# Kernel optimization log

Measured on AMD Instinct MI355X. Metric: run time of the kernel, lower is better.

Reference implementation:

```python
import jax, jax.numpy as jnp
import numpy as np

B, C, D, E = 2048, 64, 1024, 128
P_INT = 0.0  # p_int=0 -> intervention mask is all zeros (deterministic)


def setup_inputs() -> dict:
    key = jax.random.key(0)
    ks = jax.random.split(key, 16)
    s = lambda k, shape, fan: jax.random.normal(k, shape, jnp.float32) * (1.0 / np.sqrt(fan))
    return {
        "x": jax.random.normal(ks[0], (B, D), jnp.float32),
        "c_int": jax.random.uniform(ks[1], (B, C), jnp.float32),
        # stacked per-concept scorer MLP: Linear(D,D) -> ReLU -> Linear(D,1) -> Sigmoid
        "W1": s(ks[2], (C, D, D), D), "b1": jnp.zeros((C, D), jnp.float32),
        "w2": s(ks[3], (C, D), D), "b2": jnp.zeros((C,), jnp.float32),
        # stacked per-concept embed layer: Linear(D+1, D+1) -> ReLU
        "Wl": s(ks[4], (C, D + 1, D + 1), D + 1), "bl": jnp.zeros((C, D + 1), jnp.float32),
        # shared heads
        "Wmu": s(ks[5], (D + 1, E), D + 1), "bmu": jnp.zeros((E,), jnp.float32),
        "Wlv": s(ks[6], (D + 1, E), D + 1), "blv": jnp.zeros((E,), jnp.float32),
        "proto_pos": jax.random.normal(ks[7], (C, E), jnp.float32),
        "proto_neg": jax.random.normal(ks[8], (C, E), jnp.float32),
    }


def reference(x, c_int, W1, b1, w2, b2, Wl, bl, Wmu, bmu, Wlv, blv, proto_pos, proto_neg):
    # Concept scorers (all concepts batched as one grouped GEMM).
    h = jax.nn.relu(jnp.einsum("bd,cdk->bck", x, W1) + b1)          # [B,C,D]
    c_pred = jax.nn.sigmoid(jnp.einsum("bck,ck->bc", h, w2) + b2)    # [B,C]
    # Per-concept embedding layer on [x ; c_pred].
    xc = jnp.concatenate(
        [jnp.broadcast_to(x[:, None, :], (x.shape[0], C, D)), c_pred[..., None]], axis=-1
    )                                                                # [B,C,D+1]
    emb = jax.nn.relu(jnp.einsum("bck,ckj->bcj", xc, Wl) + bl)       # [B,C,D+1]
    mu = jnp.einsum("bcj,je->bce", emb, Wmu) + bmu                   # [B,C,E]
    logvar = jnp.einsum("bcj,je->bce", emb, Wlv) + blv               # [B,C,E]
    c_emb = mu  # eval mode: no reparameterization noise
    # Intervention blend (mask ~ Bernoulli(p_int); p_int=0 -> zeros, deterministic)
    mask = jnp.zeros_like(c_pred)                                    # [B,C]
    cp = mask * c_int + (1.0 - mask) * c_pred                        # [B,C]
    proto = cp[..., None] * proto_pos + (1.0 - cp[..., None]) * proto_neg  # [B,C,E]
    c_emb = mask[..., None] * proto + (1.0 - mask[..., None]) * c_emb
    return (c_pred, c_emb, mu, logvar)
```

## Files before the change

kernel.cpp:

```cpp
#include <hip/hip_runtime.h>
#include <hip/hip_bf16.h>
#include <cstdint>
#include <cstddef>

#define OFF_CE 131072ull
#define OFF_MU (131072ull + 16777216ull)
#define OFF_LV (131072ull + 33554432ull)

using bf16x8 = __attribute__((ext_vector_type(8))) __bf16;
using s16x8  = __attribute__((ext_vector_type(8))) short;
using f32x4  = __attribute__((ext_vector_type(4))) float;

__device__ __forceinline__ unsigned short f2bf(float x) {
  unsigned u = __builtin_bit_cast(unsigned, x);
  return (unsigned short)((u + 0x7FFFu + ((u >> 16) & 1u)) >> 16);
}
__device__ __forceinline__ float bf2f(unsigned short h) {
  unsigned u = ((unsigned)h) << 16;
  return __builtin_bit_cast(float, u);
}
__device__ __forceinline__ void async16(const void* g, void* l) {
  __builtin_amdgcn_global_load_lds(
      (const __attribute__((address_space(1))) void*)g,
      (__attribute__((address_space(3))) void*)l, 16, 0, 0);
}

struct P {
  const float *Wl, *bl, *Wmu, *Wlv, *b2;
  const unsigned short *xb;
  unsigned short *WlT, *WheadT;
  float *wlastf, *blpf, *Wlcolf, *w2l, *bl1024, *whead1024f, *presum, *spart, *e1024, *pred;
};

__device__ __forceinline__ void strip_transpose(const float* __restrict__ srcBase, int srcStride,
                                                unsigned short* __restrict__ dstBase, int tid,
                                                char* lds) {
  float* t64 = (float*)lds;
  const int r = tid >> 3;
  const int c8 = (tid & 7) << 3;
  for (int nc = 0; nc < 16; ++nc) {
    __syncthreads();
    const float* sp = srcBase + (size_t)r * srcStride + nc * 64 + c8;
#pragma unroll
    for (int j = 0; j < 8; ++j) t64[r * 65 + c8 + j] = sp[j];
    __syncthreads();
    unsigned short tmp[8];
#pragma unroll
    for (int j = 0; j < 8; ++j) tmp[j] = f2bf(t64[(c8 + j) * 65 + r]);
    *(uint4*)(dstBase + (size_t)(nc * 64 + r) * 1024 + c8) = *(uint4*)tmp;
  }
}

__global__ __launch_bounds__(512) void prep1_k(const float* __restrict__ W1,
                                               const float* __restrict__ x,
                                               const float* __restrict__ Wl,
                                               const float* __restrict__ bl,
                                               unsigned short* __restrict__ xb,
                                               unsigned short* __restrict__ W1T,
                                               float* __restrict__ wlastf,
                                               float* __restrict__ blpf,
                                               float* __restrict__ Wlcolf,
                                               float* __restrict__ w2l,
                                               float* __restrict__ bl1024) {
  __shared__ char lds[16640];
  const int bid = blockIdx.x;
  const int tid = threadIdx.x;
  if (bid < 1024) {
    const int c = bid & 63, k0 = (bid >> 6) << 6;
    strip_transpose(W1 + ((size_t)c << 20) + (size_t)k0 * 1024, 1024,
                    W1T + ((size_t)c << 20) + k0, tid, lds);
  } else if (bid < 1536) {
    const int idx = (bid - 1024) * 512 + tid;
    const float4* xv = (const float4*)x;
    float4 a = xv[idx * 2], b = xv[idx * 2 + 1];
    unsigned w0 = f2bf(a.x) | ((unsigned)f2bf(a.y) << 16);
    unsigned w1 = f2bf(a.z) | ((unsigned)f2bf(a.w) << 16);
    unsigned w2 = f2bf(b.x) | ((unsigned)f2bf(b.y) << 16);
    unsigned w3 = f2bf(b.z) | ((unsigned)f2bf(b.w) << 16);
    ((uint4*)xb)[idx] = make_uint4(w0, w1, w2, w3);
  } else {
    const int idx = (bid - 1536) * 512 + tid;
    const int c = idx >> 10, j = idx & 1023;
    const float* src = Wl + (size_t)c * 1050625;
    wlastf[idx] = src[(size_t)1024 * 1025 + j];
    blpf[idx]   = bl[(size_t)c * 1025 + j];
    Wlcolf[idx] = src[(size_t)j * 1025 + 1024];
    if (j == 0) {
      w2l[c]    = src[(size_t)1024 * 1025 + 1024];
      bl1024[c] = bl[(size_t)c * 1025 + 1024];
    }
  }
}

__global__ __launch_bounds__(512) void transpose_wl_strip_k(const float* __restrict__ Wl,
                                                            unsigned short* __restrict__ WlT) {
  __shared__ char lds[16640];
  const int bid = blockIdx.x;
  const int c = bid & 63, k0 = (bid >> 6) << 6;
  strip_transpose(Wl + (size_t)c * 1050625 + (size_t)k0 * 1025, 1025,
                  WlT + ((size_t)c << 20) + k0, threadIdx.x, lds);
}

template <int FUSE_WL>
__device__ void extra_work(int e, int tid, char* lds, const P& p) {
  if constexpr (FUSE_WL) {
    if (e < 1024) {
      const int c = e & 63, k0 = (e >> 6) << 6;
      strip_transpose(p.Wl + (size_t)c * 1050625 + (size_t)k0 * 1025, 1025,
                      p.WlT + ((size_t)c << 20) + k0, tid, lds);
      return;
    }
    e -= 1024;
  }
  if (e < 512) {
    const int idx = e * 512 + tid;
    const int rr = idx >> 10, k = idx & 1023;
    float v = (rr < 128) ? p.Wmu[(size_t)k * 128 + rr] : p.Wlv[(size_t)k * 128 + (rr - 128)];
    p.WheadT[idx] = f2bf(v);
    if (e == 0 && tid < 256)
      p.whead1024f[tid] = (tid < 128) ? p.Wmu[131072 + tid] : p.Wlv[131072 + (tid - 128)];
    return;
  }
  e -= 512;
  const int r0 = e << 5;
  uint4* xt4 = (uint4*)lds;
  const uint4* src4 = (const uint4*)(p.xb + ((size_t)r0 << 10));
#pragma unroll
  for (int i = 0; i < 8; ++i) xt4[tid * 8 + i] = src4[tid * 8 + i];
  __syncthreads();
  const int wv = tid >> 6, lane = tid & 63;
  const unsigned short* xt = (const unsigned short*)lds;
  for (int c = 0; c < 64; ++c) {
    float w[16];
#pragma unroll
    for (int q = 0; q < 16; ++q) w[q] = p.Wlcolf[(c << 10) + lane * 16 + q];
#pragma unroll
    for (int rr = 0; rr < 4; ++rr) {
      const int r = (wv << 2) + rr;
      const unsigned short* xr = xt + (r << 10) + lane * 16;
      float s = 0.f;
#pragma unroll
      for (int i = 0; i < 16; ++i) s += bf2f(xr[i]) * w[i];
#pragma unroll
      for (int off = 32; off; off >>= 1) s += __shfl_xor(s, off);
      if (lane == 0) p.presum[(c << 11) + r0 + r] = s;
    }
  }
}


#define BAR() __builtin_amdgcn_s_barrier()
#define LGKM0() do { asm volatile("s_waitcnt lgkmcnt(0)" ::: "memory"); \
                     __builtin_amdgcn_sched_barrier(0); } while (0)
#define VM4() asm volatile("s_waitcnt vmcnt(4)" ::: "memory")
#define VM0() asm volatile("s_waitcnt vmcnt(0)" ::: "memory")

#define STAGEA(h, tt, bidx) do { _Pragma("unroll") for (int q_ = 0; q_ < 2; ++q_) \
  async16(Asrc[q_] + ((size_t)(h) * 128) * K + (size_t)(tt) * 64, \
          &sA[bidx][(h) * 8192 + chnk[q_]]); } while (0)
#define STAGEB(h, tt, bidx) do { _Pragma("unroll") for (int q_ = 0; q_ < 2; ++q_) \
  async16(Bsrc[q_] + ((size_t)(h) * 128) * K + (size_t)(tt) * 64, \
          &sB[bidx][(h) * 8192 + chnk[q_]]); } while (0)

#define LOADA(mh, bidx) do { _Pragma("unroll") for (int i_ = 0; i_ < 4; ++i_) { \
  const int ro_ = ((mh) * 128 + wm64 + i_ * 16 + l15) << 6; \
  a[i_][0] = *(const bf16x8*)&sA[bidx][ro_ + ccx0]; \
  a[i_][1] = *(const bf16x8*)&sA[bidx][ro_ + ccx1]; } } while (0)

#define LOADB(nh, bb, bidx) do { _Pragma("unroll") for (int j_ = 0; j_ < 2; ++j_) { \
  const int ro_ = ((nh) * 128 + wn32 + j_ * 16 + l15) << 6; \
  bb[j_][0] = *(const bf16x8*)&sB[bidx][ro_ + ccx0]; \
  bb[j_][1] = *(const bf16x8*)&sB[bidx][ro_ + ccx1]; } } while (0)

#define MMAQ(mh, nh, bb) do { _Pragma("unroll") for (int i_ = 0; i_ < 4; ++i_) \
  _Pragma("unroll") for (int j_ = 0; j_ < 2; ++j_) { \
    acc[(mh)*4+i_][(nh)*2+j_] = __builtin_amdgcn_mfma_f32_16x16x32_bf16( \
        a[i_][0], bb[j_][0], acc[(mh)*4+i_][(nh)*2+j_], 0, 0, 0); \
    acc[(mh)*4+i_][(nh)*2+j_] = __builtin_amdgcn_mfma_f32_16x16x32_bf16( \
        a[i_][1], bb[j_][1], acc[(mh)*4+i_][(nh)*2+j_], 0, 0, 0); \
  } } while (0)

template <int MODE, int FUSE_WL>
__global__ __launch_bounds__(512, 2) void gemm8p_k(
    const unsigned short* __restrict__ A, const unsigned short* __restrict__ BT, const int K,
    const float* __restrict__ e0, const float* __restrict__ e1,
    const float* __restrict__ e2, const float* __restrict__ e3,
    unsigned short* __restrict__ obf, float* __restrict__ ofl, P p) {
  __shared__ unsigned short sA[2][16384];
  __shared__ unsigned short sB[2][16384];

  constexpr int GX = (MODE == 2) ? 1 : 4;
  constexpr int GY = (MODE == 2) ? 512 : 8;
  constexpr int NWG = GX * GY * ((MODE == 2) ? 1 : 64);

  const int tid = threadIdx.x;

  int rbid;
  if constexpr (MODE == 0) {
    constexpr int NE = FUSE_WL ? 1600 : 576;
    constexpr int NT = 2048 + NE;
    const int bidR = blockIdx.x;
    const int lo = (int)(((long)bidR * NE) / NT);
    const int hi = (int)(((long)(bidR + 1) * NE) / NT);
    if (hi > lo) { extra_work<FUSE_WL>(lo, tid, (char*)&sA[0][0], p); return; }
    rbid = bidR - lo;
  } else {
    rbid = blockIdx.x + GX * (blockIdx.y + GY * blockIdx.z);
  }

  const int lane = tid & 63;
  const int wid = tid >> 6;
  const int wm = wid >> 2, wn = wid & 3;
  const int l15 = lane & 15, l4 = lane >> 4;
  const int wm64 = wm << 6, wn32 = wn << 5;

  const int bid = (rbid & 7) * (NWG >> 3) + (rbid >> 3);
  const int bx = bid % GX;
  const int by = (bid / GX) % GY;
  const int c = bid / (GX * GY);

  const int n0 = bx << 8;
  const int m0 = by << 8;

  const unsigned short* Ab = A;
  const unsigned short* Bb;
  if constexpr (MODE == 2) Bb = BT;
  else                     Bb = BT + ((size_t)c << 20);

  int rloc[2], csrc[2], chnk[2];
  const unsigned short* Asrc[2];
  const unsigned short* Bsrc[2];
#pragma unroll
  for (int q = 0; q < 2; ++q) {
    const int s = ((wid << 1) + q) * 64 + lane;
    rloc[q] = s >> 3;
    csrc[q] = ((s & 7) ^ ((s >> 3) & 7)) << 3;
    chnk[q] = ((wid << 1) + q) << 9;
    Asrc[q] = Ab + (size_t)(m0 + rloc[q]) * K + csrc[q];
    Bsrc[q] = Bb + (size_t)(n0 + rloc[q]) * K + csrc[q];
  }

  const int xorv = l15 & 7;
  const int ccx0 = (l4 ^ xorv) << 3;
  const int ccx1 = ((4 + l4) ^ xorv) << 3;

  f32x4 acc[8][4];
#pragma unroll
  for (int i = 0; i < 8; ++i)
#pragma unroll
    for (int j = 0; j < 4; ++j) acc[i][j] = (f32x4)(0.f);

  bf16x8 a[4][2], b0[2][2], b1[2][2];

  const int nt = K >> 6;

  STAGEA(0, 0, 0); STAGEB(0, 0, 0); STAGEB(1, 0, 0); STAGEA(1, 0, 0);
  VM0();
  BAR();

  for (int t = 0; t < nt - 1; ++t) {
    const int cb = t & 1, nb = cb ^ 1;
    LOADA(0, cb);
    LOADB(0, b0, cb);
    STAGEA(0, t + 1, nb);
    BAR();
    LGKM0();
    __builtin_amdgcn_s_setprio(1);
    MMAQ(0, 0, b0);
    __builtin_amdgcn_s_setprio(0);
    VM4();
    BAR();
    LOADB(1, b1, cb);
    STAGEB(0, t + 1, nb);
    BAR();
    LGKM0();
    __builtin_amdgcn_s_setprio(1);
    MMAQ(0, 1, b1);
    __builtin_amdgcn_s_setprio(0);
    VM4();
    BAR();
    LOADA(1, cb);
    STAGEB(1, t + 1, nb);
    BAR();
    LGKM0();
    __builtin_amdgcn_s_setprio(1);
    MMAQ(1, 1, b1);
    __builtin_amdgcn_s_setprio(0);
    BAR();
    STAGEA(1, t + 1, nb);
    BAR();
    __builtin_amdgcn_s_setprio(1);
    MMAQ(1, 0, b0);
    __builtin_amdgcn_s_setprio(0);
    VM4();
    BAR();
  }

  {
    const int cb = (nt - 1) & 1;
    VM0();
    BAR();
    LOADA(0, cb);
    LOADB(0, b0, cb);
    LGKM0();
    __builtin_amdgcn_s_setprio(1);
    MMAQ(0, 0, b0);
    __builtin_amdgcn_s_setprio(0);
    LOADB(1, b1, cb);
    LGKM0();
    __builtin_amdgcn_s_setprio(1);
    MMAQ(0, 1, b1);
    __builtin_amdgcn_s_setprio(0);
    LOADA(1, cb);
    LGKM0();
    __builtin_amdgcn_s_setprio(1);
    MMAQ(1, 1, b1);
    MMAQ(1, 0, b0);
    __builtin_amdgcn_s_setprio(0);
  }

  int coln[2][2];
#pragma unroll
  for (int nh = 0; nh < 2; ++nh)
#pragma unroll
    for (int j = 0; j < 2; ++j) coln[nh][j] = n0 + nh * 128 + wn32 + j * 16 + l15;

  if constexpr (MODE == 0) {
    float bias[2][2], w2v[2][2];
#pragma unroll
    for (int nh = 0; nh < 2; ++nh)
#pragma unroll
      for (int j = 0; j < 2; ++j) {
        bias[nh][j] = e0[(c << 10) + coln[nh][j]];
        w2v[nh][j]  = e1[(c << 10) + coln[nh][j]];
      }
    float* partL = (float*)&sA[0][0];
#pragma unroll
    for (int mh = 0; mh < 2; ++mh)
#pragma unroll
      for (int i = 0; i < 4; ++i)
#pragma unroll
        for (int rr = 0; rr < 4; ++rr) {
          float s = 0.f;
#pragma unroll
          for (int nh = 0; nh < 2; ++nh)
#pragma unroll
            for (int j = 0; j < 2; ++j) {
              float v = fmaxf(acc[mh * 4 + i][nh * 2 + j][rr] + bias[nh][j], 0.f);
              s += v * w2v[nh][j];
            }
          s += __shfl_xor(s, 1); s += __shfl_xor(s, 2);
          s += __shfl_xor(s, 4); s += __shfl_xor(s, 8);
          if (l15 == 0) partL[wid * 128 + mh * 64 + i * 16 + (l4 << 2) + rr] = s;
        }
    __syncthreads();
    if (tid < 256) {
      const int r = tid;
      const int mh_ = r >> 7, wmr = (r >> 6) & 1, low = r & 63;
      float s2 = 0.f;
#pragma unroll
      for (int wn2 = 0; wn2 < 4; ++wn2) s2 += partL[(wmr * 4 + wn2) * 128 + mh_ * 64 + low];
      ofl[(((size_t)(bx << 6) + c) << 11) + m0 + r] = s2;
    }
  } else if constexpr (MODE == 1) {
    float* cpL = (float*)&sA[0][0];
    if (tid < 256) {
      const int b = m0 + tid;
      float s = p.b2[c];
#pragma unroll
      for (int q = 0; q < 4; ++q) s += e2[(((size_t)(q << 6) + c) << 11) + b];
      float pv = 1.f / (1.f + expf(-s));
      cpL[tid] = pv;
      if (bx == 0) {
        p.pred[((size_t)b << 6) + c] = pv;
        p.e1024[(c << 11) + b] =
            fmaxf(p.presum[(c << 11) + b] + pv * p.w2l[c] + p.bl1024[c], 0.f);
      }
    }
    __syncthreads();
    float wl4[2][2], bb4[2][2];
#pragma unroll
    for (int nh = 0; nh < 2; ++nh)
#pragma unroll
      for (int j = 0; j < 2; ++j) {
        wl4[nh][j] = e0[(c << 10) + coln[nh][j]];
        bb4[nh][j] = e1[(c << 10) + coln[nh][j]];
      }
#pragma unroll
    for (int mh = 0; mh < 2; ++mh)
#pragma unroll
      for (int i = 0; i < 4; ++i)
#pragma unroll
        for (int rr = 0; rr < 4; ++rr) {
          const int rl = mh * 128 + wm64 + i * 16 + (l4 << 2) + rr;
          const int row = m0 + rl;
          const float cp = cpL[rl];
          unsigned short* orow = obf + (((size_t)(c << 11) + row) << 10);
#pragma unroll
          for (int nh = 0; nh < 2; ++nh)
#pragma unroll
            for (int j = 0; j < 2; ++j) {
              float v = acc[mh * 4 + i][nh * 2 + j][rr] + cp * wl4[nh][j] + bb4[nh][j];
              orow[coln[nh][j]] = f2bf(fmaxf(v, 0.f));
            }
        }
  } else {
    float bias[2][2], wh[2][2];
#pragma unroll
    for (int nh = 0; nh < 2; ++nh)
#pragma unroll
      for (int j = 0; j < 2; ++j) {
        bias[nh][j] = (nh == 0) ? e0[coln[0][j]] : e1[coln[1][j] - 128];
        wh[nh][j]   = e3[coln[nh][j]];
      }
#pragma unroll
    for (int mh = 0; mh < 2; ++mh)
#pragma unroll
      for (int i = 0; i < 4; ++i)
#pragma unroll
        for (int rr = 0; rr < 4; ++rr) {
          const int rid = m0 + mh * 128 + wm64 + i * 16 + (l4 << 2) + rr;
          const int cc = rid >> 11, b = rid & 2047;
          const float ev = e2[rid];
          const size_t ib = (((size_t)b << 6) + cc) << 7;
#pragma unroll
          for (int j = 0; j < 2; ++j) {
            float v = acc[mh * 4 + i][j][rr] + bias[0][j] + ev * wh[0][j];
            ofl[OFF_MU + ib + coln[0][j]] = v;
            ofl[OFF_CE + ib + coln[0][j]] = v;
          }
#pragma unroll
          for (int j = 0; j < 2; ++j) {
            float v = acc[mh * 4 + i][2 + j][rr] + bias[1][j] + ev * wh[1][j];
            ofl[OFF_LV + ib + (coln[1][j] - 128)] = v;
          }
        }
  }
}


extern "C" void kernel_launch(void* const* d_in, const int* in_sizes, int n_in,
                              void* d_out, int out_size, void* d_ws, size_t ws_size,
                              hipStream_t stream) {
  const float* x   = (const float*)d_in[0];
  const float* W1  = (const float*)d_in[2];
  const float* b1  = (const float*)d_in[3];
  const float* w2  = (const float*)d_in[4];
  const float* b2  = (const float*)d_in[5];
  const float* Wl  = (const float*)d_in[6];
  const float* bl  = (const float*)d_in[7];
  const float* Wmu = (const float*)d_in[8];
  const float* bmu = (const float*)d_in[9];
  const float* Wlv = (const float*)d_in[10];
  const float* blv = (const float*)d_in[11];
  float* out = (float*)d_out;

  const bool fuse = ws_size >= 545523712ull;

  char* ws = (char*)d_ws;
  size_t off = 0;
  auto take = [&](size_t bytes) { char* r = ws + off; off += bytes; return r; };
  unsigned short* xb     = (unsigned short*)take(4194304);
  unsigned short* W1T    = (unsigned short*)take(134217728);
  unsigned short* WlT    = fuse ? (unsigned short*)take(134217728) : W1T;
  float* wlastf          = (float*)take(262144);
  float* blpf            = (float*)take(262144);
  float* Wlcolf          = (float*)take(262144);
  float* w2l             = (float*)take(512);
  float* bl1024          = (float*)take(512);
  unsigned short* WheadT = (unsigned short*)take(524288);
  float* whead1024f      = (float*)take(1024);
  float* presum          = (float*)take(524288);
  float* spart           = (float*)take(2097152);
  float* e1024f          = (float*)take(524288);
  unsigned short* emb    = (unsigned short*)take(268435456);

  P p;
  p.Wl = Wl; p.bl = bl; p.Wmu = Wmu; p.Wlv = Wlv; p.b2 = b2;
  p.xb = xb; p.WlT = WlT; p.WheadT = WheadT;
  p.wlastf = wlastf; p.blpf = blpf; p.Wlcolf = Wlcolf; p.w2l = w2l; p.bl1024 = bl1024;
  p.whead1024f = whead1024f; p.presum = presum; p.spart = spart;
  p.e1024 = e1024f; p.pred = out;

  prep1_k<<<1664, 512, 0, stream>>>(W1, x, Wl, bl, xb, W1T, wlastf, blpf, Wlcolf, w2l, bl1024);
  if (fuse) {
    gemm8p_k<0, 1><<<2048 + 1600, 512, 0, stream>>>(xb, W1T, 1024, b1, w2, nullptr, nullptr,
                                                    nullptr, spart, p);
  } else {
    gemm8p_k<0, 0><<<2048 + 576, 512, 0, stream>>>(xb, W1T, 1024, b1, w2, nullptr, nullptr,
                                                   nullptr, spart, p);
    transpose_wl_strip_k<<<1024, 512, 0, stream>>>(Wl, WlT);
  }
  gemm8p_k<1, 0><<<dim3(4, 8, 64), 512, 0, stream>>>(xb, WlT, 1024, wlastf, blpf, spart, nullptr,
                                                     emb, nullptr, p);
  gemm8p_k<2, 0><<<dim3(1, 512, 1), 512, 0, stream>>>(emb, WheadT, 1024, bmu, blv, e1024f,
                                                      whead1024f, nullptr, out, p);
}
```

Measured before the change: 1.137 ms.

## Replace strip transposes with 64x64 tile kernels and unfuse extra work from GEMM

Weight transposes now use one 256-thread block per 64x64 tile with float4 loads (for W1), replacing the serial 16-step strip loop. The extra work that used to be interleaved into the first GEMM grid (Wl transpose, head weight transpose, presum dot products) moves to a separate wl2_k kernel launched between the two grouped GEMMs. This lets one transposed-weight buffer be reused for W1 and Wl. presum is recomputed with one block per row using vector loads. The cost is losing the overlap of transpose work with GEMM compute, in exchange for better-parallelised, more coalesced transposes.

```diff
diff --git a/kernel.cpp b/kernel.cpp
--- a/kernel.cpp
+++ b/kernel.cpp
@@ -25,33 +25,41 @@
       (__attribute__((address_space(3))) void*)l, 16, 0, 0);
 }
 
-struct P {
-  const float *Wl, *bl, *Wmu, *Wlv, *b2;
-  const unsigned short *xb;
-  unsigned short *WlT, *WheadT;
-  float *wlastf, *blpf, *Wlcolf, *w2l, *bl1024, *whead1024f, *presum, *spart, *e1024, *pred;
+struct P2 {
+  const float *b2, *presum, *w2l, *bl1024;
+  float *e1024, *pred;
 };
 
-__device__ __forceinline__ void strip_transpose(const float* __restrict__ srcBase, int srcStride,
-                                                unsigned short* __restrict__ dstBase, int tid,
-                                                char* lds) {
-  float* t64 = (float*)lds;
-  const int r = tid >> 3;
-  const int c8 = (tid & 7) << 3;
-  for (int nc = 0; nc < 16; ++nc) {
-    __syncthreads();
-    const float* sp = srcBase + (size_t)r * srcStride + nc * 64 + c8;
-#pragma unroll
-    for (int j = 0; j < 8; ++j) t64[r * 65 + c8 + j] = sp[j];
-    __syncthreads();
+template <int ALIGNED>
+__device__ __forceinline__ void tile_tr64(const float* __restrict__ src, int stride,
+                                          unsigned short* __restrict__ dst, int tid,
+                                          float (*t)[68]) {
+#pragma unroll
+  for (int i = 0; i < 4; ++i) {
+    const int row = (tid >> 4) + (i << 4);
+    const int col4 = (tid & 15) << 2;
+    const float* sp = src + (size_t)row * stride + col4;
+    float4 v;
+    if constexpr (ALIGNED) {
+      v = *(const float4*)sp;
+    } else {
+      v.x = sp[0]; v.y = sp[1]; v.z = sp[2]; v.w = sp[3];
+    }
+    *(float4*)&t[row][col4] = v;
+  }
+  __syncthreads();
+  const int n = tid & 63;
+#pragma unroll
+  for (int p = 0; p < 2; ++p) {
+    const int k8 = ((tid >> 6) << 3) + (p << 5);
     unsigned short tmp[8];
 #pragma unroll
-    for (int j = 0; j < 8; ++j) tmp[j] = f2bf(t64[(c8 + j) * 65 + r]);
-    *(uint4*)(dstBase + (size_t)(nc * 64 + r) * 1024 + c8) = *(uint4*)tmp;
-  }
-}
-
-__global__ __launch_bounds__(512) void prep1_k(const float* __restrict__ W1,
+    for (int j = 0; j < 8; ++j) tmp[j] = f2bf(t[k8 + j][n]);
+    *(uint4*)(dst + (size_t)n * 1024 + k8) = *(uint4*)tmp;
+  }
+}
+
+__global__ __launch_bounds__(256) void prep1_k(const float* __restrict__ W1,
                                                const float* __restrict__ x,
                                                const float* __restrict__ Wl,
                                                const float* __restrict__ bl,
@@ -62,15 +70,15 @@
                                                float* __restrict__ Wlcolf,
                                                float* __restrict__ w2l,
                                                float* __restrict__ bl1024) {
-  __shared__ char lds[16640];
+  __shared__ float t[64][68];
   const int bid = blockIdx.x;
   const int tid = threadIdx.x;
-  if (bid < 1024) {
-    const int c = bid & 63, k0 = (bid >> 6) << 6;
-    strip_transpose(W1 + ((size_t)c << 20) + (size_t)k0 * 1024, 1024,
-                    W1T + ((size_t)c << 20) + k0, tid, lds);
-  } else if (bid < 1536) {
-    const int idx = (bid - 1024) * 512 + tid;
+  if (bid < 16384) {
+    const int c = bid >> 8, kt = (bid >> 4) & 15, nt = bid & 15;
+    tile_tr64<1>(W1 + ((size_t)c << 20) + ((size_t)(kt << 6) << 10) + (nt << 6), 1024,
+                 W1T + ((size_t)c << 20) + ((size_t)(nt << 6) << 10) + (kt << 6), tid, t);
+  } else if (bid < 17408) {
+    const int idx = (bid - 16384) * 256 + tid;
     const float4* xv = (const float4*)x;
     float4 a = xv[idx * 2], b = xv[idx * 2 + 1];
     unsigned w0 = f2bf(a.x) | ((unsigned)f2bf(a.y) << 16);
@@ -79,7 +87,7 @@
     unsigned w3 = f2bf(b.z) | ((unsigned)f2bf(b.w) << 16);
     ((uint4*)xb)[idx] = make_uint4(w0, w1, w2, w3);
   } else {
-    const int idx = (bid - 1536) * 512 + tid;
+    const int idx = (bid - 17408) * 256 + tid;
     const int c = idx >> 10, j = idx & 1023;
     const float* src = Wl + (size_t)c * 1050625;
     wlastf[idx] = src[(size_t)1024 * 1025 + j];
@@ -92,58 +100,56 @@
   }
 }
 
-__global__ __launch_bounds__(512) void transpose_wl_strip_k(const float* __restrict__ Wl,
-                                                            unsigned short* __restrict__ WlT) {
-  __shared__ char lds[16640];
+__global__ __launch_bounds__(256) void wl2_k(const float* __restrict__ Wl,
+                                             const float* __restrict__ Wmu,
+                                             const float* __restrict__ Wlv,
+                                             const unsigned short* __restrict__ xb,
+                                             const float* __restrict__ Wlcolf,
+                                             unsigned short* __restrict__ WlT,
+                                             unsigned short* __restrict__ WheadT,
+                                             float* __restrict__ whead1024f,
+                                             float* __restrict__ presum) {
+  __shared__ float t[64][68];
   const int bid = blockIdx.x;
-  const int c = bid & 63, k0 = (bid >> 6) << 6;
-  strip_transpose(Wl + (size_t)c * 1050625 + (size_t)k0 * 1025, 1025,
-                  WlT + ((size_t)c << 20) + k0, threadIdx.x, lds);
-}
-
-template <int FUSE_WL>
-__device__ void extra_work(int e, int tid, char* lds, const P& p) {
-  if constexpr (FUSE_WL) {
-    if (e < 1024) {
-      const int c = e & 63, k0 = (e >> 6) << 6;
-      strip_transpose(p.Wl + (size_t)c * 1050625 + (size_t)k0 * 1025, 1025,
-                      p.WlT + ((size_t)c << 20) + k0, tid, lds);
-      return;
-    }
-    e -= 1024;
-  }
-  if (e < 512) {
-    const int idx = e * 512 + tid;
+  const int tid = threadIdx.x;
+  if (bid < 16384) {
+    const int c = bid >> 8, kt = (bid >> 4) & 15, nt = bid & 15;
+    tile_tr64<0>(Wl + (size_t)c * 1050625 + (size_t)(kt << 6) * 1025 + (nt << 6), 1025,
+                 WlT + ((size_t)c << 20) + ((size_t)(nt << 6) << 10) + (kt << 6), tid, t);
+  } else if (bid < 17408) {
+    const int e = bid - 16384;
+    const int idx = e * 256 + tid;
     const int rr = idx >> 10, k = idx & 1023;
-    float v = (rr < 128) ? p.Wmu[(size_t)k * 128 + rr] : p.Wlv[(size_t)k * 128 + (rr - 128)];
-    p.WheadT[idx] = f2bf(v);
-    if (e == 0 && tid < 256)
-      p.whead1024f[tid] = (tid < 128) ? p.Wmu[131072 + tid] : p.Wlv[131072 + (tid - 128)];
-    return;
-  }
-  e -= 512;
-  const int r0 = e << 5;
-  uint4* xt4 = (uint4*)lds;
-  const uint4* src4 = (const uint4*)(p.xb + ((size_t)r0 << 10));
-#pragma unroll
-  for (int i = 0; i < 8; ++i) xt4[tid * 8 + i] = src4[tid * 8 + i];
-  __syncthreads();
-  const int wv = tid >> 6, lane = tid & 63;
-  const unsigned short* xt = (const unsigned short*)lds;
-  for (int c = 0; c < 64; ++c) {
-    float w[16];
-#pragma unroll
-    for (int q = 0; q < 16; ++q) w[q] = p.Wlcolf[(c << 10) + lane * 16 + q];
-#pragma unroll
-    for (int rr = 0; rr < 4; ++rr) {
-      const int r = (wv << 2) + rr;
-      const unsigned short* xr = xt + (r << 10) + lane * 16;
+    float v = (rr < 128) ? Wmu[(size_t)k * 128 + rr] : Wlv[(size_t)k * 128 + (rr - 128)];
+    WheadT[idx] = f2bf(v);
+    if (e == 0)
+      whead1024f[tid] = (tid < 128) ? Wmu[131072 + tid] : Wlv[131072 + (tid - 128)];
+  } else {
+    const int b = bid - 17408;
+    const int w = tid >> 6, lane = tid & 63;
+    const unsigned short* xr = xb + ((size_t)b << 10) + lane * 16;
+    s16x8 xv0 = *(const s16x8*)xr;
+    s16x8 xv1 = *(const s16x8*)(xr + 8);
+    float xf[16];
+#pragma unroll
+    for (int i = 0; i < 8; ++i) {
+      xf[i] = bf2f((unsigned short)xv0[i]);
+      xf[8 + i] = bf2f((unsigned short)xv1[i]);
+    }
+#pragma unroll
+    for (int t16 = 0; t16 < 16; ++t16) {
+      const int c = (t16 << 2) + w;
+      const float* wr = Wlcolf + (c << 10) + lane * 16;
       float s = 0.f;
 #pragma unroll
-      for (int i = 0; i < 16; ++i) s += bf2f(xr[i]) * w[i];
+      for (int q = 0; q < 4; ++q) {
+        float4 wv = *(const float4*)(wr + q * 4);
+        s += xf[q * 4 + 0] * wv.x + xf[q * 4 + 1] * wv.y +
+             xf[q * 4 + 2] * wv.z + xf[q * 4 + 3] * wv.w;
+      }
 #pragma unroll
       for (int off = 32; off; off >>= 1) s += __shfl_xor(s, off);
-      if (lane == 0) p.presum[(c << 11) + r0 + r] = s;
+      if (lane == 0) presum[(c << 11) + b] = s;
     }
   }
 }
@@ -180,12 +186,12 @@
         a[i_][1], bb[j_][1], acc[(mh)*4+i_][(nh)*2+j_], 0, 0, 0); \
   } } while (0)
 
-template <int MODE, int FUSE_WL>
+template <int MODE>
 __global__ __launch_bounds__(512, 2) void gemm8p_k(
     const unsigned short* __restrict__ A, const unsigned short* __restrict__ BT, const int K,
     const float* __restrict__ e0, const float* __restrict__ e1,
     const float* __restrict__ e2, const float* __restrict__ e3,
-    unsigned short* __restrict__ obf, float* __restrict__ ofl, P p) {
+    unsigned short* __restrict__ obf, float* __restrict__ ofl, P2 p) {
   __shared__ unsigned short sA[2][16384];
   __shared__ unsigned short sB[2][16384];
 
@@ -194,26 +200,13 @@
   constexpr int NWG = GX * GY * ((MODE == 2) ? 1 : 64);
 
   const int tid = threadIdx.x;
-
-  int rbid;
-  if constexpr (MODE == 0) {
-    constexpr int NE = FUSE_WL ? 1600 : 576;
-    constexpr int NT = 2048 + NE;
-    const int bidR = blockIdx.x;
-    const int lo = (int)(((long)bidR * NE) / NT);
-    const int hi = (int)(((long)(bidR + 1) * NE) / NT);
-    if (hi > lo) { extra_work<FUSE_WL>(lo, tid, (char*)&sA[0][0], p); return; }
-    rbid = bidR - lo;
-  } else {
-    rbid = blockIdx.x + GX * (blockIdx.y + GY * blockIdx.z);
-  }
-
   const int lane = tid & 63;
   const int wid = tid >> 6;
   const int wm = wid >> 2, wn = wid & 3;
   const int l15 = lane & 15, l4 = lane >> 4;
   const int wm64 = wm << 6, wn32 = wn << 5;
 
+  const int rbid = blockIdx.x + GX * (blockIdx.y + GY * blockIdx.z);
   const int bid = (rbid & 7) * (NWG >> 3) + (rbid >> 3);
   const int bx = bid % GX;
   const int by = (bid / GX) % GY;
@@ -455,14 +448,11 @@
   const float* blv = (const float*)d_in[11];
   float* out = (float*)d_out;
 
-  const bool fuse = ws_size >= 545523712ull;
-
   char* ws = (char*)d_ws;
   size_t off = 0;
   auto take = [&](size_t bytes) { char* r = ws + off; off += bytes; return r; };
   unsigned short* xb     = (unsigned short*)take(4194304);
-  unsigned short* W1T    = (unsigned short*)take(134217728);
-  unsigned short* WlT    = fuse ? (unsigned short*)take(134217728) : W1T;
+  unsigned short* WT     = (unsigned short*)take(134217728);
   float* wlastf          = (float*)take(262144);
   float* blpf            = (float*)take(262144);
   float* Wlcolf          = (float*)take(262144);
@@ -475,24 +465,16 @@
   float* e1024f          = (float*)take(524288);
   unsigned short* emb    = (unsigned short*)take(268435456);
 
-  P p;
-  p.Wl = Wl; p.bl = bl; p.Wmu = Wmu; p.Wlv = Wlv; p.b2 = b2;
-  p.xb = xb; p.WlT = WlT; p.WheadT = WheadT;
-  p.wlastf = wlastf; p.blpf = blpf; p.Wlcolf = Wlcolf; p.w2l = w2l; p.bl1024 = bl1024;
-  p.whead1024f = whead1024f; p.presum = presum; p.spart = spart;
+  P2 p;
+  p.b2 = b2; p.presum = presum; p.w2l = w2l; p.bl1024 = bl1024;
   p.e1024 = e1024f; p.pred = out;
 
-  prep1_k<<<1664, 512, 0, stream>>>(W1, x, Wl, bl, xb, W1T, wlastf, blpf, Wlcolf, w2l, bl1024);
-  if (fuse) {
-    gemm8p_k<0, 1><<<2048 + 1600, 512, 0, stream>>>(xb, W1T, 1024, b1, w2, nullptr, nullptr,
-                                                    nullptr, spart, p);
-  } else {
-    gemm8p_k<0, 0><<<2048 + 576, 512, 0, stream>>>(xb, W1T, 1024, b1, w2, nullptr, nullptr,
-                                                   nullptr, spart, p);
-    transpose_wl_strip_k<<<1024, 512, 0, stream>>>(Wl, WlT);
-  }
-  gemm8p_k<1, 0><<<dim3(4, 8, 64), 512, 0, stream>>>(xb, WlT, 1024, wlastf, blpf, spart, nullptr,
-                                                     emb, nullptr, p);
-  gemm8p_k<2, 0><<<dim3(1, 512, 1), 512, 0, stream>>>(emb, WheadT, 1024, bmu, blv, e1024f,
-                                                      whead1024f, nullptr, out, p);
-}
+  prep1_k<<<17664, 256, 0, stream>>>(W1, x, Wl, bl, xb, WT, wlastf, blpf, Wlcolf, w2l, bl1024);
+  gemm8p_k<0><<<dim3(4, 8, 64), 512, 0, stream>>>(xb, WT, 1024, b1, w2, nullptr, nullptr,
+                                                  nullptr, spart, p);
+  wl2_k<<<19456, 256, 0, stream>>>(Wl, Wmu, Wlv, xb, Wlcolf, WT, WheadT, whead1024f, presum);
+  gemm8p_k<1><<<dim3(4, 8, 64), 512, 0, stream>>>(xb, WT, 1024, wlastf, blpf, spart, nullptr,
+                                                  emb, nullptr, p);
+  gemm8p_k<2><<<dim3(1, 512, 1), 512, 0, stream>>>(emb, WheadT, 1024, bmu, blv, e1024f,
+                                                   whead1024f, nullptr, out, p);
+}
```

New measurement: 992.1 us. 12.7% less time.
